# Kernel optimization log

Hardware: AMD Instinct MI355X
Metric: run time of the kernel (lower is better)

Reference implementation:

```python
import jax, jax.numpy as jnp
import numpy as np

B, T, H = 8, 2048, 1024
P = 64           # num_attention_project
N = 4096         # config.n (bias table length), N >= 2T-1
WINDOW = 64      # relative_attention
NEG = -10000.0


def setup_inputs() -> dict:
    key = jax.random.key(0)
    ks = jax.random.split(key, 10)
    s = 1.0 / np.sqrt(H)
    sp = 1.0 / np.sqrt(P)
    sb = 1.0 / np.sqrt(N)
    return {
        "attn_input": jax.random.normal(ks[0], (B, T, H), dtype=jnp.float32),
        "attention_mask": jnp.ones((B, T), dtype=jnp.float32),
        # Linear weights stored as [in, out] so y = x @ W + b
        "Wq": jax.random.uniform(ks[1], (H, P), minval=-s, maxval=s),
        "bq": jnp.zeros((P,), jnp.float32),
        "Wk": jax.random.uniform(ks[2], (H, P), minval=-s, maxval=s),
        "bk": jnp.zeros((P,), jnp.float32),
        "Wv": jax.random.uniform(ks[3], (H, P), minval=-s, maxval=s),
        "bv": jnp.zeros((P,), jnp.float32),
        "Wo": jax.random.uniform(ks[4], (P, H), minval=-sp, maxval=sp),
        "bo": jnp.zeros((H,), jnp.float32),
        "bias": jax.random.uniform(ks[5], (N,), minval=-sb, maxval=sb),
    }


def reference(attn_input, attention_mask, Wq, bq, Wk, bk, Wv, bv, Wo, bo, bias):
    q = attn_input @ Wq + bq            # [B,T,P]
    k = attn_input @ Wk + bk
    v = attn_input @ Wv + bv
    scores = jnp.einsum("btp,bsp->bts", q, k) / jnp.sqrt(jnp.float32(P))  # [B,T,T]
    # padding mask: note original broadcasts over COLUMNS via unsqueeze(-1)
    scores = scores + (1.0 - attention_mask)[:, :, None] * NEG
    # circulant window mask: keep |i-j| <= WINDOW (all ones if WINDOW >= T)
    i = jnp.arange(T)
    rel = i[:, None] - i[None, :]       # i - j
    win = (jnp.abs(rel) <= WINDOW) | (WINDOW >= T)
    scores = scores + jnp.where(win, 0.0, NEG)[None, :, :]
    # gathered learnable relative-position bias: bias[n//2 - i + j]
    scores = scores + bias[N // 2 - rel][None, :, :]
    attn = jax.nn.softmax(scores, axis=-1)
    out = jnp.einsum("bts,bsp->btp", attn, v)
    return out @ Wo + bo                # [B,T,H]
```

## Files before the change

kernel.cpp:

```cpp
#include <hip/hip_runtime.h>

using bf16x8 = __attribute__((ext_vector_type(8))) short;
using f32x4  = __attribute__((ext_vector_type(4))) float;

static __device__ inline unsigned short f2bf(float f) {
  unsigned int u = __float_as_uint(f);
  u += 0x7fffu + ((u >> 16) & 1u);
  return (unsigned short)(u >> 16);
}
static __device__ inline unsigned int pk2(float a, float b) {
  return (unsigned int)f2bf(a) | ((unsigned int)f2bf(b) << 16);
}

#define ROW16_MAX(x) { \
  { int _t = __builtin_amdgcn_update_dpp(0, __float_as_int(x), 0x121, 0xf, 0xf, true); x = fmaxf(x, __int_as_float(_t)); } \
  { int _t = __builtin_amdgcn_update_dpp(0, __float_as_int(x), 0x122, 0xf, 0xf, true); x = fmaxf(x, __int_as_float(_t)); } \
  { int _t = __builtin_amdgcn_update_dpp(0, __float_as_int(x), 0x124, 0xf, 0xf, true); x = fmaxf(x, __int_as_float(_t)); } \
  { int _t = __builtin_amdgcn_update_dpp(0, __float_as_int(x), 0x128, 0xf, 0xf, true); x = fmaxf(x, __int_as_float(_t)); } }
#define ROW16_SUM(x) { \
  { int _t = __builtin_amdgcn_update_dpp(0, __float_as_int(x), 0x121, 0xf, 0xf, true); x += __int_as_float(_t); } \
  { int _t = __builtin_amdgcn_update_dpp(0, __float_as_int(x), 0x122, 0xf, 0xf, true); x += __int_as_float(_t); } \
  { int _t = __builtin_amdgcn_update_dpp(0, __float_as_int(x), 0x124, 0xf, 0xf, true); x += __int_as_float(_t); } \
  { int _t = __builtin_amdgcn_update_dpp(0, __float_as_int(x), 0x128, 0xf, 0xf, true); x += __int_as_float(_t); } }

__global__ __launch_bounds__(256) void prep_kernel(
    const float* __restrict__ Wq, const float* __restrict__ Wk, const float* __restrict__ Wv,
    const float* __restrict__ Wo, const float* __restrict__ bq, const float* __restrict__ bk,
    const float* __restrict__ bv,
    unsigned short* __restrict__ Wt, unsigned short* __restrict__ Wot, float* __restrict__ bqkv)
{
  int idx = blockIdx.x * 256 + threadIdx.x;
  if (idx < 192 * 1024) {
    int n = idx >> 10, k = idx & 1023;
    const float* W = (n < 64) ? Wq : (n < 128) ? Wk : Wv;
    Wt[idx] = f2bf(W[k * 64 + (n & 63)]);
  } else if (idx < 192 * 1024 + 1024 * 64) {
    int j = idx - 192 * 1024;
    int n = j >> 6, k = j & 63;
    Wot[j] = f2bf(Wo[k * 1024 + n]);
  } else if (idx < 192 * 1024 + 1024 * 64 + 192) {
    int n = idx - (192 * 1024 + 1024 * 64);
    bqkv[n] = (n < 64) ? bq[n] : (n < 128) ? bk[n - 64] : bv[n - 128];
  }
}

#define QKV_STORE(BUF, A0, A1, B0, B1, B2) { \
  uint4 pv_; \
  pv_.x = pk2(A0.x, A0.y); pv_.y = pk2(A0.z, A0.w); \
  pv_.z = pk2(A1.x, A1.y); pv_.w = pk2(A1.z, A1.w); \
  *(uint4*)(As[BUF] + rowA * 72 + cA * 8) = pv_; \
  *(uint4*)(Bs[BUF] + rowA * 72 + cA * 8) = B0; \
  *(uint4*)(Bs[BUF] + (rowA + 32) * 72 + cA * 8) = B1; \
  *(uint4*)(Bs[BUF] + (rowA + 64) * 72 + cA * 8) = B2; }

#define QKV_LOAD(KS, A0, A1, B0, B1, B2) { \
  const float* sA_ = srcA + (KS) * 64; \
  A0 = *(const float4*)(sA_); A1 = *(const float4*)(sA_ + 4); \
  const unsigned short* sB_ = srcB + (KS) * 64; \
  B0 = *(const uint4*)(sB_); \
  B1 = *(const uint4*)(sB_ + 32 * 1024); \
  B2 = *(const uint4*)(sB_ + 64 * 1024); }

#define QKV_MMA(BUF) { \
  _Pragma("unroll") \
  for (int kk = 0; kk < 64; kk += 32) { \
    int ko = kk + quad * 8; \
    bf16x8 afr = *(const bf16x8*)(As[BUF] + (mg * 16 + col) * 72 + ko); \
    _Pragma("unroll") \
    for (int ns = 0; ns < 3; ++ns) { \
      bf16x8 bfr = *(const bf16x8*)(Bs[BUF] + ((ng * 3 + ns) * 16 + col) * 72 + ko); \
      acc[ns] = __builtin_amdgcn_mfma_f32_16x16x32_bf16(afr, bfr, acc[ns], 0, 0, 0); \
    } } }

__global__ __launch_bounds__(256) void qkv_gemm(
    const float* __restrict__ X, const unsigned short* __restrict__ Wt,
    const float* __restrict__ bqkv, unsigned short* __restrict__ qkvb)
{
  __shared__ __align__(16) unsigned short As[2][32 * 72];
  __shared__ __align__(16) unsigned short Bs[2][96 * 72];
  int t = threadIdx.x;
  int lane = t & 63, w = t >> 6;
  int m0 = (blockIdx.x >> 1) * 32;
  int nbase = (blockIdx.x & 1) * 96;
  int mg = w & 1, ng = w >> 1;
  int col = lane & 15, quad = lane >> 4;
  f32x4 acc[3] = {};

  int rowA = t >> 3, cA = t & 7;
  const float* srcA = X + (size_t)(m0 + rowA) * 1024 + cA * 8;
  const unsigned short* srcB = Wt + (size_t)(nbase + rowA) * 1024 + cA * 8;

  float4 eA0, eA1; uint4 eB0, eB1, eB2;
  float4 oA0, oA1; uint4 oB0, oB1, oB2;
  QKV_LOAD(0, eA0, eA1, eB0, eB1, eB2);
  QKV_LOAD(1, oA0, oA1, oB0, oB1, oB2);

  for (int ks = 0; ks < 16; ks += 2) {
    QKV_STORE(0, eA0, eA1, eB0, eB1, eB2);
    if (ks + 2 < 16) QKV_LOAD(ks + 2, eA0, eA1, eB0, eB1, eB2);
    __syncthreads();
    QKV_MMA(0);
    QKV_STORE(1, oA0, oA1, oB0, oB1, oB2);
    if (ks + 3 < 16) QKV_LOAD(ks + 3, oA0, oA1, oB0, oB1, oB2);
    __syncthreads();
    QKV_MMA(1);
  }
  #pragma unroll
  for (int ns = 0; ns < 3; ++ns)
    #pragma unroll
    for (int r = 0; r < 4; ++r) {
      int m = m0 + mg * 16 + quad * 4 + r;
      int n = nbase + ng * 48 + ns * 16 + col;
      qkvb[(size_t)m * 192 + n] = f2bf(acc[ns][r] + bqkv[n]);
    }
}

__global__ __launch_bounds__(512) void band_attn(
    const unsigned short* __restrict__ qkvb, const float* __restrict__ bias,
    unsigned short* __restrict__ attnout)
{
  __shared__ __align__(16) unsigned short Kl[192 * 72];
  __shared__ __align__(16) unsigned short Vt[64 * 216];
  __shared__ __align__(16) unsigned short Ps[4 * 16 * 168];
  __shared__ float Osum[4][16][64];
  __shared__ float Mx[8][16];
  __shared__ float Lx[8][16];
  __shared__ float biasL[129];

  int t = threadIdx.x;
  int lane = t & 63, w = t >> 6;
  int p = w >> 1, s = w & 1;
  int col = lane & 15, quad = lane >> 4, q4 = quad * 4;
  int bidx = blockIdx.x;
  int b = bidx >> 5;
  int i0 = (bidx & 31) * 64;
  int jw = i0 - 64;
  const unsigned short* qbase = qkvb + (size_t)(b << 11) * 192;

  int iq = i0 + p * 16;
  const unsigned short* qr = qbase + (size_t)(iq + col) * 192 + quad * 8;
  bf16x8 aq0 = *(const bf16x8*)(qr);
  bf16x8 aq1 = *(const bf16x8*)(qr + 32);

  if (t < 129) biasL[t] = bias[1984 + t];
  #pragma unroll
  for (int it = 0; it < 6; ++it) {
    int idx = it * 512 + t;
    int row = idx >> 4;
    int c = idx & 15;
    int jb = jw + row;
    int jc = jb < 0 ? 0 : (jb > 2047 ? 2047 : jb);
    const unsigned short* src = qbase + (size_t)jc * 192 + 64 + c * 8;
    uint4 v = *(const uint4*)src;
    if (c < 8) {
      *(uint4*)(Kl + row * 72 + c * 8) = v;
    } else {
      union { uint4 u; unsigned short ss[8]; } uv; uv.u = v;
      int p0 = (c - 8) * 8;
      #pragma unroll
      for (int e = 0; e < 8; ++e) Vt[(p0 + e) * 216 + row] = uv.ss[e];
    }
  }
  if (t < 256) {
    int pz = t >> 2, c0 = 192 + (t & 3) * 4;
    *(uint2*)(Vt + pz * 216 + c0) = make_uint2(0u, 0u);
  }
  __syncthreads();

  int nt9 = 5 - s, t9b = 5 * s;
  f32x4 sv[5];
  for (int i = 0; i < nt9; ++i) {
    int t9 = t9b + i;
    int krow = ((p + t9) * 16 + col) * 72;
    bf16x8 kb0 = *(const bf16x8*)(Kl + krow + quad * 8);
    bf16x8 kb1 = *(const bf16x8*)(Kl + krow + 32 + quad * 8);
    f32x4 z = {};
    z = __builtin_amdgcn_mfma_f32_16x16x32_bf16(aq0, kb0, z, 0, 0, 0);
    sv[i] = __builtin_amdgcn_mfma_f32_16x16x32_bf16(aq1, kb1, z, 0, 0, 0);
  }
  float mrow[4] = {-3e38f, -3e38f, -3e38f, -3e38f};
  for (int i = 0; i < nt9; ++i) {
    int t9 = t9b + i;
    int j = iq - 64 + t9 * 16 + col;
    #pragma unroll
    for (int r = 0; r < 4; ++r) {
      int diff = q4 + r + 64 - t9 * 16 - col;
      bool valid = (j >= 0) & (j < 2048) & (diff >= -64) & (diff <= 64);
      int bi = 64 - diff; bi = bi < 0 ? 0 : (bi > 128 ? 128 : bi);
      float x = valid ? (sv[i][r] * 0.125f + biasL[bi]) : -3e38f;
      sv[i][r] = x;
      mrow[r] = fmaxf(mrow[r], x);
    }
  }
  #pragma unroll
  for (int r = 0; r < 4; ++r) ROW16_MAX(mrow[r]);
  if (col == 0) {
    #pragma unroll
    for (int r = 0; r < 4; ++r) Mx[w][q4 + r] = mrow[r];
  }
  __syncthreads();
  #pragma unroll
  for (int r = 0; r < 4; ++r) mrow[r] = fmaxf(mrow[r], Mx[w ^ 1][q4 + r]);

  unsigned short* Pw = Ps + p * (16 * 168);
  float lsum[4] = {0.f, 0.f, 0.f, 0.f};
  for (int i = 0; i < nt9; ++i) {
    int t9 = t9b + i;
    #pragma unroll
    for (int r = 0; r < 4; ++r) {
      float pe = __expf(sv[i][r] - mrow[r]);
      lsum[r] += pe;
      Pw[(q4 + r) * 168 + t9 * 16 + col] = f2bf(pe);
    }
  }
  #pragma unroll
  for (int r = 0; r < 4; ++r) ROW16_SUM(lsum[r]);
  if (col == 0) {
    #pragma unroll
    for (int r = 0; r < 4; ++r) Lx[w][q4 + r] = lsum[r];
  }
  if (s == 0) {
    #pragma unroll
    for (int r = 0; r < 4; ++r) Pw[(q4 + r) * 168 + 144 + col] = 0;
  }
  __syncthreads();
  #pragma unroll
  for (int r = 0; r < 4; ++r) lsum[r] += Lx[w ^ 1][q4 + r];

  f32x4 o[4] = {};
  int nkc = 3 - s, kcb = 3 * s;
  for (int i = 0; i < nkc; ++i) {
    int kc = kcb + i;
    bf16x8 pa = *(const bf16x8*)(Pw + col * 168 + kc * 32 + quad * 8);
    #pragma unroll
    for (int nt = 0; nt < 4; ++nt) {
      bf16x8 vb = *(const bf16x8*)(Vt + (nt * 16 + col) * 216 + 16 * p + kc * 32 + quad * 8);
      o[nt] = __builtin_amdgcn_mfma_f32_16x16x32_bf16(pa, vb, o[nt], 0, 0, 0);
    }
  }
  if (s == 1) {
    #pragma unroll
    for (int nt = 0; nt < 4; ++nt)
      #pragma unroll
      for (int r = 0; r < 4; ++r)
        Osum[p][q4 + r][nt * 16 + col] = o[nt][r];
  }
  __syncthreads();
  if (s == 0) {
    float rl[4];
    #pragma unroll
    for (int r = 0; r < 4; ++r) rl[r] = 1.0f / lsum[r];
    #pragma unroll
    for (int nt = 0; nt < 4; ++nt)
      #pragma unroll
      for (int r = 0; r < 4; ++r) {
        int arow = (b << 11) + iq + q4 + r;
        attnout[(size_t)arow * 64 + nt * 16 + col] =
            f2bf((o[nt][r] + Osum[p][q4 + r][nt * 16 + col]) * rl[r]);
      }
  }
}

__global__ __launch_bounds__(256) void out_gemm(
    const unsigned short* __restrict__ attn, const unsigned short* __restrict__ Wot,
    const float* __restrict__ bo, float* __restrict__ out)
{
  __shared__ __align__(16) unsigned short As[64 * 72];
  __shared__ __align__(16) unsigned short Bs[128 * 72];
  int t = threadIdx.x, lane = t & 63, w = t >> 6;
  int m0 = (blockIdx.x >> 3) * 64;
  int n0 = (blockIdx.x & 7) * 128;
  #pragma unroll
  for (int r = 0; r < 2; ++r) {
    int tau = t + 256 * r; int row = tau >> 3, c = tau & 7;
    *(uint4*)(As + row * 72 + c * 8) =
        *(const uint4*)(attn + (size_t)(m0 + row) * 64 + c * 8);
  }
  #pragma unroll
  for (int r = 0; r < 4; ++r) {
    int tau = t + 256 * r; int n = tau >> 3, c = tau & 7;
    *(uint4*)(Bs + n * 72 + c * 8) =
        *(const uint4*)(Wot + (size_t)(n0 + n) * 64 + c * 8);
  }
  __syncthreads();
  f32x4 acc[2][4] = {};
  int mg = w & 1, ngg = w >> 1;
  #pragma unroll
  for (int kk = 0; kk < 64; kk += 32) {
    int ko = kk + (lane >> 4) * 8;
    bf16x8 a0 = *(const bf16x8*)(As + (mg * 32 +      (lane & 15)) * 72 + ko);
    bf16x8 a1 = *(const bf16x8*)(As + (mg * 32 + 16 + (lane & 15)) * 72 + ko);
    #pragma unroll
    for (int ns = 0; ns < 4; ++ns) {
      bf16x8 b = *(const bf16x8*)(Bs + ((ngg * 4 + ns) * 16 + (lane & 15)) * 72 + ko);
      acc[0][ns] = __builtin_amdgcn_mfma_f32_16x16x32_bf16(a0, b, acc[0][ns], 0, 0, 0);
      acc[1][ns] = __builtin_amdgcn_mfma_f32_16x16x32_bf16(a1, b, acc[1][ns], 0, 0, 0);
    }
  }
  int col = lane & 15, q = lane >> 4;
  #pragma unroll
  for (int ms = 0; ms < 2; ++ms)
    #pragma unroll
    for (int ns = 0; ns < 4; ++ns)
      #pragma unroll
      for (int r = 0; r < 4; ++r) {
        int mm = m0 + mg * 32 + ms * 16 + q * 4 + r;
        int nn = n0 + (ngg * 4 + ns) * 16 + col;
        out[(size_t)mm * 1024 + nn] = acc[ms][ns][r] + bo[nn];
      }
}

extern "C" void kernel_launch(void* const* d_in, const int* in_sizes, int n_in,
                              void* d_out, int out_size, void* d_ws, size_t ws_size,
                              hipStream_t stream) {
  const float* X    = (const float*)d_in[0];
  const float* Wq   = (const float*)d_in[2];
  const float* bq   = (const float*)d_in[3];
  const float* Wk   = (const float*)d_in[4];
  const float* bk   = (const float*)d_in[5];
  const float* Wv   = (const float*)d_in[6];
  const float* bv   = (const float*)d_in[7];
  const float* Wo   = (const float*)d_in[8];
  const float* bo   = (const float*)d_in[9];
  const float* bias = (const float*)d_in[10];
  float* out = (float*)d_out;
  char* ws = (char*)d_ws;
  unsigned short* qkvb = (unsigned short*)(ws);
  unsigned short* attn = (unsigned short*)(ws + 6291456);
  unsigned short* Wt   = (unsigned short*)(ws + 8388608);
  unsigned short* Wot  = (unsigned short*)(ws + 8781824);
  float*          bqkv = (float*)(ws + 8912896);

  prep_kernel<<<1025, 256, 0, stream>>>(Wq, Wk, Wv, Wo, bq, bk, bv, Wt, Wot, bqkv);
  qkv_gemm<<<1024, 256, 0, stream>>>(X, Wt, bqkv, qkvb);
  band_attn<<<256, 512, 0, stream>>>(qkvb, bias, attn);
  out_gemm<<<2048, 256, 0, stream>>>(attn, Wot, bo, out);
}
```

Before: 167.5 us.

## Fuse output projection into band attention and widen QKV GEMM tiles to all outputs

The output projection (attn @ Wo + bo) moves into the attention kernel. Each block converts its normalized 64x64 attention output to bf16 in shared memory, and each of its 8 waves computes a 128-column slice of the 1024-wide output with MFMA. This removes the separate out_gemm launch and the global round trip of the intermediate attention tensor. Separately, the QKV GEMM now gives each block all 192 output columns for a 32-row tile, halving the grid to 512 blocks and reading X once instead of twice, at the cost of more registers and LDS per block. The fused output stage runs on only 256 blocks, so writing the large fp32 output may be less parallel than before.

New measurement: 228.0 us. 1.36x slower.

```diff
diff --git a/kernel.cpp b/kernel.cpp
--- a/kernel.cpp
+++ b/kernel.cpp
@@ -44,22 +44,21 @@
   }
 }
 
-#define QKV_STORE(BUF, A0, A1, B0, B1, B2) { \
+#define QKV_LOAD(KS, A0, A1, B) { \
+  const float* sA_ = srcA + (KS) * 64; \
+  A0 = *(const float4*)(sA_); A1 = *(const float4*)(sA_ + 4); \
+  const unsigned short* sB_ = srcB + (KS) * 64; \
+  _Pragma("unroll") \
+  for (int r_ = 0; r_ < 6; ++r_) B[r_] = *(const uint4*)(sB_ + (size_t)r_ * 32 * 1024); }
+
+#define QKV_STORE(BUF, A0, A1, B) { \
   uint4 pv_; \
   pv_.x = pk2(A0.x, A0.y); pv_.y = pk2(A0.z, A0.w); \
   pv_.z = pk2(A1.x, A1.y); pv_.w = pk2(A1.z, A1.w); \
   *(uint4*)(As[BUF] + rowA * 72 + cA * 8) = pv_; \
-  *(uint4*)(Bs[BUF] + rowA * 72 + cA * 8) = B0; \
-  *(uint4*)(Bs[BUF] + (rowA + 32) * 72 + cA * 8) = B1; \
-  *(uint4*)(Bs[BUF] + (rowA + 64) * 72 + cA * 8) = B2; }
-
-#define QKV_LOAD(KS, A0, A1, B0, B1, B2) { \
-  const float* sA_ = srcA + (KS) * 64; \
-  A0 = *(const float4*)(sA_); A1 = *(const float4*)(sA_ + 4); \
-  const unsigned short* sB_ = srcB + (KS) * 64; \
-  B0 = *(const uint4*)(sB_); \
-  B1 = *(const uint4*)(sB_ + 32 * 1024); \
-  B2 = *(const uint4*)(sB_ + 64 * 1024); }
+  _Pragma("unroll") \
+  for (int r_ = 0; r_ < 6; ++r_) \
+    *(uint4*)(Bs[BUF] + (rowA + 32 * r_) * 72 + cA * 8) = B[r_]; }
 
 #define QKV_MMA(BUF) { \
   _Pragma("unroll") \
@@ -67,8 +66,8 @@
     int ko = kk + quad * 8; \
     bf16x8 afr = *(const bf16x8*)(As[BUF] + (mg * 16 + col) * 72 + ko); \
     _Pragma("unroll") \
-    for (int ns = 0; ns < 3; ++ns) { \
-      bf16x8 bfr = *(const bf16x8*)(Bs[BUF] + ((ng * 3 + ns) * 16 + col) * 72 + ko); \
+    for (int ns = 0; ns < 6; ++ns) { \
+      bf16x8 bfr = *(const bf16x8*)(Bs[BUF] + ((ng * 6 + ns) * 16 + col) * 72 + ko); \
       acc[ns] = __builtin_amdgcn_mfma_f32_16x16x32_bf16(afr, bfr, acc[ns], 0, 0, 0); \
     } } }
 
@@ -77,51 +76,52 @@
     const float* __restrict__ bqkv, unsigned short* __restrict__ qkvb)
 {
   __shared__ __align__(16) unsigned short As[2][32 * 72];
-  __shared__ __align__(16) unsigned short Bs[2][96 * 72];
+  __shared__ __align__(16) unsigned short Bs[2][192 * 72];
   int t = threadIdx.x;
   int lane = t & 63, w = t >> 6;
-  int m0 = (blockIdx.x >> 1) * 32;
-  int nbase = (blockIdx.x & 1) * 96;
+  int m0 = blockIdx.x * 32;
   int mg = w & 1, ng = w >> 1;
   int col = lane & 15, quad = lane >> 4;
-  f32x4 acc[3] = {};
+  f32x4 acc[6] = {};
 
   int rowA = t >> 3, cA = t & 7;
   const float* srcA = X + (size_t)(m0 + rowA) * 1024 + cA * 8;
-  const unsigned short* srcB = Wt + (size_t)(nbase + rowA) * 1024 + cA * 8;
-
-  float4 eA0, eA1; uint4 eB0, eB1, eB2;
-  float4 oA0, oA1; uint4 oB0, oB1, oB2;
-  QKV_LOAD(0, eA0, eA1, eB0, eB1, eB2);
-  QKV_LOAD(1, oA0, oA1, oB0, oB1, oB2);
+  const unsigned short* srcB = Wt + (size_t)rowA * 1024 + cA * 8;
+
+  float4 eA0, eA1; uint4 eB[6];
+  float4 oA0, oA1; uint4 oB[6];
+  QKV_LOAD(0, eA0, eA1, eB);
+  QKV_LOAD(1, oA0, oA1, oB);
 
   for (int ks = 0; ks < 16; ks += 2) {
-    QKV_STORE(0, eA0, eA1, eB0, eB1, eB2);
-    if (ks + 2 < 16) QKV_LOAD(ks + 2, eA0, eA1, eB0, eB1, eB2);
+    QKV_STORE(0, eA0, eA1, eB);
+    if (ks + 2 < 16) QKV_LOAD(ks + 2, eA0, eA1, eB);
     __syncthreads();
     QKV_MMA(0);
-    QKV_STORE(1, oA0, oA1, oB0, oB1, oB2);
-    if (ks + 3 < 16) QKV_LOAD(ks + 3, oA0, oA1, oB0, oB1, oB2);
+    QKV_STORE(1, oA0, oA1, oB);
+    if (ks + 3 < 16) QKV_LOAD(ks + 3, oA0, oA1, oB);
     __syncthreads();
     QKV_MMA(1);
   }
   #pragma unroll
-  for (int ns = 0; ns < 3; ++ns)
+  for (int ns = 0; ns < 6; ++ns)
     #pragma unroll
     for (int r = 0; r < 4; ++r) {
       int m = m0 + mg * 16 + quad * 4 + r;
-      int n = nbase + ng * 48 + ns * 16 + col;
+      int n = ng * 96 + ns * 16 + col;
       qkvb[(size_t)m * 192 + n] = f2bf(acc[ns][r] + bqkv[n]);
     }
 }
 
-__global__ __launch_bounds__(512) void band_attn(
+__global__ __launch_bounds__(512) void attn_out(
     const unsigned short* __restrict__ qkvb, const float* __restrict__ bias,
-    unsigned short* __restrict__ attnout)
+    const unsigned short* __restrict__ Wot, const float* __restrict__ bo,
+    float* __restrict__ out)
 {
   __shared__ __align__(16) unsigned short Kl[192 * 72];
   __shared__ __align__(16) unsigned short Vt[64 * 216];
   __shared__ __align__(16) unsigned short Ps[4 * 16 * 168];
+  __shared__ __align__(16) unsigned short Obf[64 * 72];
   __shared__ float Osum[4][16][64];
   __shared__ float Mx[8][16];
   __shared__ float Lx[8][16];
@@ -253,61 +253,39 @@
     #pragma unroll
     for (int nt = 0; nt < 4; ++nt)
       #pragma unroll
-      for (int r = 0; r < 4; ++r) {
-        int arow = (b << 11) + iq + q4 + r;
-        attnout[(size_t)arow * 64 + nt * 16 + col] =
+      for (int r = 0; r < 4; ++r)
+        Obf[(p * 16 + q4 + r) * 72 + nt * 16 + col] =
             f2bf((o[nt][r] + Osum[p][q4 + r][nt * 16 + col]) * rl[r]);
-      }
-  }
-}
-
-__global__ __launch_bounds__(256) void out_gemm(
-    const unsigned short* __restrict__ attn, const unsigned short* __restrict__ Wot,
-    const float* __restrict__ bo, float* __restrict__ out)
-{
-  __shared__ __align__(16) unsigned short As[64 * 72];
-  __shared__ __align__(16) unsigned short Bs[128 * 72];
-  int t = threadIdx.x, lane = t & 63, w = t >> 6;
-  int m0 = (blockIdx.x >> 3) * 64;
-  int n0 = (blockIdx.x & 7) * 128;
-  #pragma unroll
-  for (int r = 0; r < 2; ++r) {
-    int tau = t + 256 * r; int row = tau >> 3, c = tau & 7;
-    *(uint4*)(As + row * 72 + c * 8) =
-        *(const uint4*)(attn + (size_t)(m0 + row) * 64 + c * 8);
-  }
-  #pragma unroll
-  for (int r = 0; r < 4; ++r) {
-    int tau = t + 256 * r; int n = tau >> 3, c = tau & 7;
-    *(uint4*)(Bs + n * 72 + c * 8) =
-        *(const uint4*)(Wot + (size_t)(n0 + n) * 64 + c * 8);
-  }
-  __syncthreads();
-  f32x4 acc[2][4] = {};
-  int mg = w & 1, ngg = w >> 1;
-  #pragma unroll
-  for (int kk = 0; kk < 64; kk += 32) {
-    int ko = kk + (lane >> 4) * 8;
-    bf16x8 a0 = *(const bf16x8*)(As + (mg * 32 +      (lane & 15)) * 72 + ko);
-    bf16x8 a1 = *(const bf16x8*)(As + (mg * 32 + 16 + (lane & 15)) * 72 + ko);
-    #pragma unroll
-    for (int ns = 0; ns < 4; ++ns) {
-      bf16x8 b = *(const bf16x8*)(Bs + ((ngg * 4 + ns) * 16 + (lane & 15)) * 72 + ko);
-      acc[0][ns] = __builtin_amdgcn_mfma_f32_16x16x32_bf16(a0, b, acc[0][ns], 0, 0, 0);
-      acc[1][ns] = __builtin_amdgcn_mfma_f32_16x16x32_bf16(a1, b, acc[1][ns], 0, 0, 0);
-    }
-  }
-  int col = lane & 15, q = lane >> 4;
-  #pragma unroll
-  for (int ms = 0; ms < 2; ++ms)
-    #pragma unroll
-    for (int ns = 0; ns < 4; ++ns)
+  }
+  __syncthreads();
+
+  const unsigned short* wb_base = Wot + (size_t)(w * 128 + col) * 64 + quad * 8;
+  bf16x8 wb[8][2];
+  #pragma unroll
+  for (int ns = 0; ns < 8; ++ns) {
+    wb[ns][0] = *(const bf16x8*)(wb_base + ns * 16 * 64);
+    wb[ns][1] = *(const bf16x8*)(wb_base + ns * 16 * 64 + 32);
+  }
+  float bov[8];
+  #pragma unroll
+  for (int ns = 0; ns < 8; ++ns) bov[ns] = bo[w * 128 + ns * 16 + col];
+  float* outbase = out + ((size_t)(b << 11) + i0) * 1024 + w * 128;
+  #pragma unroll
+  for (int mt = 0; mt < 4; ++mt) {
+    bf16x8 a0 = *(const bf16x8*)(Obf + (mt * 16 + col) * 72 + quad * 8);
+    bf16x8 a1 = *(const bf16x8*)(Obf + (mt * 16 + col) * 72 + 32 + quad * 8);
+    f32x4 acc8[8] = {};
+    #pragma unroll
+    for (int ns = 0; ns < 8; ++ns) {
+      acc8[ns] = __builtin_amdgcn_mfma_f32_16x16x32_bf16(a0, wb[ns][0], acc8[ns], 0, 0, 0);
+      acc8[ns] = __builtin_amdgcn_mfma_f32_16x16x32_bf16(a1, wb[ns][1], acc8[ns], 0, 0, 0);
+    }
+    #pragma unroll
+    for (int ns = 0; ns < 8; ++ns)
       #pragma unroll
-      for (int r = 0; r < 4; ++r) {
-        int mm = m0 + mg * 32 + ms * 16 + q * 4 + r;
-        int nn = n0 + (ngg * 4 + ns) * 16 + col;
-        out[(size_t)mm * 1024 + nn] = acc[ms][ns][r] + bo[nn];
-      }
+      for (int r = 0; r < 4; ++r)
+        outbase[(size_t)(mt * 16 + q4 + r) * 1024 + ns * 16 + col] = acc8[ns][r] + bov[ns];
+  }
 }
 
 extern "C" void kernel_launch(void* const* d_in, const int* in_sizes, int n_in,
@@ -326,13 +304,11 @@
   float* out = (float*)d_out;
   char* ws = (char*)d_ws;
   unsigned short* qkvb = (unsigned short*)(ws);
-  unsigned short* attn = (unsigned short*)(ws + 6291456);
-  unsigned short* Wt   = (unsigned short*)(ws + 8388608);
-  unsigned short* Wot  = (unsigned short*)(ws + 8781824);
-  float*          bqkv = (float*)(ws + 8912896);
+  unsigned short* Wt   = (unsigned short*)(ws + 6291456);
+  unsigned short* Wot  = (unsigned short*)(ws + 6684672);
+  float*          bqkv = (float*)(ws + 6815744);
 
   prep_kernel<<<1025, 256, 0, stream>>>(Wq, Wk, Wv, Wo, bq, bk, bv, Wt, Wot, bqkv);
-  qkv_gemm<<<1024, 256, 0, stream>>>(X, Wt, bqkv, qkvb);
-  band_attn<<<256, 512, 0, stream>>>(qkvb, bias, attn);
-  out_gemm<<<2048, 256, 0, stream>>>(attn, Wot, bo, out);
-}
+  qkv_gemm<<<512, 256, 0, stream>>>(X, Wt, bqkv, qkvb);
+  attn_out<<<256, 512, 0, stream>>>(qkvb, bias, Wot, bo, out);
+}
```
